# Performance work log

Hardware: AMD Instinct MI355X
Metric: run time of the kernel (lower is better)

The kernel has to match this reference:

```python
import jax, jax.numpy as jnp
import numpy as np

D_MODEL, D_K, D_V, H = 1024, 64, 64, 16
B, NQ, NK = 4, 2048, 2048


def setup_inputs() -> dict:
    key = jax.random.key(0)
    ks = jax.random.split(key, 14)
    def xavier(k, fan_in, fan_out):
        lim = np.sqrt(6.0 / (fan_in + fan_out))
        return jax.random.uniform(k, (fan_in, fan_out), jnp.float32, -lim, lim)
    return {
        "queries": jax.random.normal(ks[0], (B, NQ, D_MODEL), jnp.float32),
        "keys": jax.random.normal(ks[1], (B, NK, D_MODEL), jnp.float32),
        "values": jax.random.normal(ks[2], (B, NK, D_MODEL), jnp.float32),
        "language_feature": jax.random.normal(ks[3], (B, NQ, D_MODEL), jnp.float32),
        "Wq": xavier(ks[4], D_MODEL, H * D_K), "bq": jnp.zeros((H * D_K,), jnp.float32),
        "Wk": xavier(ks[5], D_MODEL, H * D_K), "bk": jnp.zeros((H * D_K,), jnp.float32),
        "Wv": xavier(ks[6], D_MODEL, H * D_V), "bv": jnp.zeros((H * D_V,), jnp.float32),
        "Ws": xavier(ks[7], D_MODEL, H * D_K), "bs": jnp.zeros((H * D_K,), jnp.float32),
        "Wo": xavier(ks[8], H * D_V, D_MODEL), "bo": jnp.zeros((D_MODEL,), jnp.float32),
    }


def reference(queries, keys, values, language_feature, Wq, bq, Wk, bk, Wv, bv, Ws, bs, Wo, bo):
    b, nq = queries.shape[:2]
    nk = keys.shape[1]
    scale = 1.0 / np.sqrt(D_K)
    # projections -> [b, h, n, d]
    q = (queries @ Wq + bq).reshape(b, nq, H, D_K).transpose(0, 2, 1, 3)
    s = (language_feature @ Ws + bs).reshape(b, nq, H, D_K).transpose(0, 2, 1, 3)
    k = (keys @ Wk + bk).reshape(b, nk, H, D_K).transpose(0, 2, 1, 3)
    v = (values @ Wv + bv).reshape(b, nk, H, D_V).transpose(0, 2, 1, 3)
    # raw scaled scores [b, h, nq, nk]
    att = jnp.einsum("bhqd,bhkd->bhqk", q, k) * scale
    # language branch: per-query dot(q_i, s_i) -> [b, h, nq]
    lang = jnp.einsum("bhqd,bhqd->bhq", q, s) * scale
    # concatenated softmax over [nk + 1]; only last column (beta) is used
    combined = jax.nn.softmax(jnp.concatenate([att, lang[..., None]], axis=-1), axis=-1)
    beta = combined[..., -1:]  # [b, h, nq, 1]
    # NOTE: original uses RAW (non-softmaxed) att for the value aggregation
    att_v = jnp.einsum("bhqk,bhkd->bhqd", att, v)
    out = beta * s + (1.0 - beta) * att_v  # [b, h, nq, d]
    out = out.transpose(0, 2, 1, 3).reshape(b, nq, H * D_V)
    return out @ Wo + bo
```

## Files before the change

kernel.cpp:

```cpp
#include <hip/hip_runtime.h>


#define SCALE 0.125f
#define LOG2E 1.44269504088896f
#define SCLOG 0.18033688011112042f

typedef __attribute__((ext_vector_type(8))) short bf16x8;
typedef __attribute__((ext_vector_type(4))) short s16x4;
typedef __attribute__((ext_vector_type(4))) float f32x4;

__device__ __forceinline__ float b2f(short x) {
  return __uint_as_float(((unsigned)(unsigned short)x) << 16);
}
__device__ __forceinline__ short f2b(float x) {
  unsigned u = __float_as_uint(x);
  unsigned r = (u + 0x7fffu + ((u >> 16) & 1u)) >> 16;
  return (short)r;
}
__device__ __forceinline__ float fexp2(float x) {
  float r;
  asm("v_exp_f32 %0, %1" : "=v"(r) : "v"(x));
  return r;
}

__device__ __forceinline__ void gl2lds16(const short* g, short* l) {
  __builtin_amdgcn_global_load_lds(
      (const __attribute__((address_space(1))) unsigned int*)g,
      (__attribute__((address_space(3))) unsigned int*)l, 16, 0, 0);
}

__global__ __launch_bounds__(256) void a2b_kernel(const float* I0, const float* I1,
                                                  const float* I2, const float* I3,
                                                  short* O0, short* O1, short* O2, short* O3) {
  const float* Ip[4] = {I0, I1, I2, I3};
  short* Op[4] = {O0, O1, O2, O3};
  const float* I = Ip[blockIdx.z];
  short* O = Op[blockIdx.z];
  const size_t n = (size_t)8192 * 1024;
  size_t stride = (size_t)gridDim.x * 256 * 8;
  for (size_t i = ((size_t)blockIdx.x * 256 + threadIdx.x) * 8; i < n; i += stride) {
    f32x4 v0 = *reinterpret_cast<const f32x4*>(&I[i]);
    f32x4 v1 = *reinterpret_cast<const f32x4*>(&I[i + 4]);
    bf16x8 o;
    for (int j = 0; j < 4; ++j) { o[j] = f2b(v0[j]); o[j + 4] = f2b(v1[j]); }
    *reinterpret_cast<bf16x8*>(&O[i]) = o;
  }
}

__global__ __launch_bounds__(256) void wtrans_kernel(
    const float* W0, const float* W1, const float* W2, const float* W3, const float* W4,
    short* O0, short* O1, short* O2, short* O3, short* O4) {
  const float* Wp[5] = {W0, W1, W2, W3, W4};
  short* Op[5] = {O0, O1, O2, O3, O4};
  const float* W = Wp[blockIdx.z];
  short* O = Op[blockIdx.z];
  int n0 = blockIdx.x * 64, k0 = blockIdx.y * 64;
  __shared__ float ts[64 * 68];
  int tid = threadIdx.x;
  int r = tid >> 4, c = (tid & 15) * 4;
  for (int ir = 0; ir < 4; ++ir) {
    f32x4 v = *reinterpret_cast<const f32x4*>(&W[(size_t)(k0 + r + ir * 16) * 1024 + n0 + c]);
    *reinterpret_cast<f32x4*>(&ts[(r + ir * 16) * 68 + c]) = v;
  }
  __syncthreads();
  for (int ir = 0; ir < 4; ++ir) {
    int n = r + ir * 16;
    s16x4 o;
    for (int j = 0; j < 4; ++j) o[j] = f2b(ts[(c + j) * 68 + n]);
    *reinterpret_cast<s16x4*>(&O[(size_t)(n0 + n) * 1024 + k0 + c]) = o;
  }
}

#define GEMM_STAGE_HALF(T, HALF)                                            \
  {                                                                         \
    int kst = (T) * 32;                                                     \
    int sb = (T) & 3;                                                       \
    short* Ad = &AsAll[sb * 8192];                                          \
    short* Bd = &BsAll[sb * 8192];                                          \
    int s = tid + (HALF) * 512;                                             \
    int row = s >> 2, cc = s & 3;                                           \
    int gc = (cc ^ ((row >> 1) & 3)) * 8;                                   \
    gl2lds16(&Ag[(size_t)(m0 + row) * 1024 + kst + gc], &Ad[s * 8]);        \
    gl2lds16(&Bg[(size_t)(n0 + row) * 1024 + kst + gc], &Bd[s * 8]);        \
  }

#define GEMM_STAGE(T) { GEMM_STAGE_HALF(T, 0); GEMM_STAGE_HALF(T, 1); }

#define GEMM_BODY(T, DO_STAGE, VM)                                          \
  {                                                                         \
    const int bi = (T) & 3;                                                 \
    const short* Ab = &AsAll[bi * 8192];                                    \
    const short* Bb = &BsAll[bi * 8192];                                    \
    bf16x8 a[4], b[4];                                                      \
    _Pragma("unroll") for (int i = 0; i < 4; ++i) {                         \
      int r = wr + i * 16 + lr;                                             \
      a[i] = *reinterpret_cast<const bf16x8*>(                              \
          &Ab[r * 32 + ((lg ^ ((r >> 1) & 3)) * 8)]);                       \
    }                                                                       \
    _Pragma("unroll") for (int j = 0; j < 4; ++j) {                         \
      int rn = wc + j * 16 + lr;                                            \
      b[j] = *reinterpret_cast<const bf16x8*>(                              \
          &Bb[rn * 32 + ((lg ^ ((rn >> 1) & 3)) * 8)]);                     \
    }                                                                       \
    if (DO_STAGE) GEMM_STAGE_HALF((T) + 3, 0);                              \
    __builtin_amdgcn_s_setprio(1);                                          \
    _Pragma("unroll") for (int j = 0; j < 4; ++j)                           \
      _Pragma("unroll") for (int i = 0; i < 4; ++i)                         \
        acc[i][j] = __builtin_amdgcn_mfma_f32_16x16x32_bf16(a[i], b[j], acc[i][j], 0, 0, 0); \
    __builtin_amdgcn_s_setprio(0);                                          \
    __builtin_amdgcn_s_barrier();                                           \
    bf16x8 a2[4];                                                           \
    _Pragma("unroll") for (int i = 0; i < 4; ++i) {                         \
      int r = wr + 64 + i * 16 + lr;                                        \
      a2[i] = *reinterpret_cast<const bf16x8*>(                             \
          &Ab[r * 32 + ((lg ^ ((r >> 1) & 3)) * 8)]);                       \
    }                                                                       \
    if (DO_STAGE) GEMM_STAGE_HALF((T) + 3, 1);                              \
    asm volatile("s_waitcnt vmcnt(" #VM ")" ::: "memory");                  \
    __builtin_amdgcn_s_setprio(1);                                          \
    _Pragma("unroll") for (int j = 0; j < 4; ++j)                           \
      _Pragma("unroll") for (int i = 0; i < 4; ++i)                         \
        acc[i + 4][j] = __builtin_amdgcn_mfma_f32_16x16x32_bf16(a2[i], b[j], acc[i + 4][j], 0, 0, 0); \
    __builtin_amdgcn_s_setprio(0);                                          \
    __builtin_amdgcn_s_barrier();                                           \
  }

#define GEMM_CORE()                                                         \
  GEMM_STAGE(0); GEMM_STAGE(1); GEMM_STAGE(2);                              \
  asm volatile("s_waitcnt vmcnt(8)" ::: "memory");                          \
  __builtin_amdgcn_s_barrier();                                             \
  for (int t = 0; t < 29; ++t) GEMM_BODY(t, true, 8);                       \
  GEMM_BODY(29, false, 4);                                                  \
  GEMM_BODY(30, false, 0);                                                  \
  GEMM_BODY(31, false, 0);

__global__ __launch_bounds__(512, 2) void proj_gemm_kernel(
    const short* A0, const short* A1, const short* A2, const short* A3,
    const short* W0, const short* W1, const short* W2, const short* W3,
    const float* c0, const float* c1, const float* c2, const float* c3,
    short* O0, short* O1, short* O2, short* O3) {
  const short* Ap[4] = {A0, A1, A2, A3};
  const short* Wp[4] = {W0, W1, W2, W3};
  const float* bp[4] = {c0, c1, c2, c3};
  short* Op[4] = {O0, O1, O2, O3};

  int id = blockIdx.x;
  int work = (id & 7) * 64 + (id >> 3);
  int z = work >> 7;
  int rem = work & 127;
  int my = rem >> 2;
  int nx = rem & 3;
  const short* Ag = Ap[z];
  const short* Bg = Wp[z];
  const float* bias = bp[z];
  short* Out = Op[z];
  int m0 = my * 256, n0 = nx * 256;

  __shared__ short AsAll[4 * 8192];
  __shared__ short BsAll[4 * 8192];
  int tid = threadIdx.x;
  int wave = tid >> 6, lane = tid & 63, lg = lane >> 4, lr = lane & 15;
  int wr = (wave >> 2) * 128, wc = (wave & 3) * 64;

  f32x4 acc[8][4] = {};

  GEMM_CORE();

#pragma unroll
  for (int j = 0; j < 4; ++j) {
    int n = n0 + wc + j * 16 + lr;
    float bi = bias[n];
    int hh = n >> 6, d = n & 63;
#pragma unroll
    for (int i = 0; i < 8; ++i)
      for (int rr = 0; rr < 4; ++rr) {
        int m = m0 + wr + i * 16 + lg * 4 + rr;
        int bb = m >> 11, t = m & 2047;
        Out[(size_t)(((bb << 4) + hh) * 2048 + t) * 64 + d] = f2b(acc[i][j][rr] + bi);
      }
  }
}

__global__ __launch_bounds__(256) void final_gemm_kernel(const short* A, const short* Wt,
                                                         const float* bias, float* Out) {
  int id = blockIdx.x;
  int work = (id & 7) * 64 + (id >> 3);
  int my = work >> 3, nx = work & 7;
  int m0 = my * 128, n0 = nx * 128;

  __shared__ short As[128 * 64];
  __shared__ short Bs[128 * 64];
  int tid = threadIdx.x;
  int wave = tid >> 6, lane = tid & 63, lg = lane >> 4, lr = lane & 15;
  int wr = (wave >> 1) * 64, wc = (wave & 1) * 64;
  f32x4 acc[4][4] = {};
  int srow = lane >> 3, scol = (lane & 7) * 8;

  for (int k0 = 0; k0 < 1024; k0 += 64) {
    __syncthreads();
#pragma unroll
    for (int i = 0; i < 4; ++i) {
      int c = i * 4 + wave;
      gl2lds16(&A[(size_t)(m0 + c * 8 + srow) * 1024 + k0 + scol], &As[c * 512 + lane * 8]);
      gl2lds16(&Wt[(size_t)(n0 + c * 8 + srow) * 1024 + k0 + scol], &Bs[c * 512 + lane * 8]);
    }
    __syncthreads();
#pragma unroll
    for (int kk = 0; kk < 2; ++kk) {
      bf16x8 a[4], b[4];
      for (int i = 0; i < 4; ++i)
        a[i] = *reinterpret_cast<const bf16x8*>(&As[(wr + i * 16 + lr) * 64 + kk * 32 + lg * 8]);
      for (int j = 0; j < 4; ++j)
        b[j] = *reinterpret_cast<const bf16x8*>(&Bs[(wc + j * 16 + lr) * 64 + kk * 32 + lg * 8]);
      for (int i = 0; i < 4; ++i)
        for (int j = 0; j < 4; ++j)
          acc[i][j] = __builtin_amdgcn_mfma_f32_16x16x32_bf16(a[i], b[j], acc[i][j], 0, 0, 0);
    }
  }
  for (int j = 0; j < 4; ++j) {
    int n = n0 + wc + j * 16 + lr;
    float bi = bias[n];
    for (int i = 0; i < 4; ++i)
      for (int rr = 0; rr < 4; ++rr) {
        int m = m0 + wr + i * 16 + lg * 4 + rr;
        Out[(size_t)m * 1024 + n] = acc[i][j][rr] + bi;
      }
  }
}

__global__ __launch_bounds__(256) void kv_kernel(const short* Kp, const short* Vp, float* KVp) {
  int c = blockIdx.x, bh = blockIdx.y;
  int tid = threadIdx.x;
  __shared__ float Ks[32 * 64];
  __shared__ float Vs[32 * 64];
  int srow = tid >> 3, scol = (tid & 7) * 8;
  int dk = tid >> 2, dv0 = (tid & 3) * 16;
  float acc[16] = {};
  for (int sub = 0; sub < 8; ++sub) {
    int tkb = c * 256 + sub * 32;
    __syncthreads();
    bf16x8 kv = *reinterpret_cast<const bf16x8*>(&Kp[(size_t)(bh * 2048 + tkb + srow) * 64 + scol]);
    bf16x8 vv = *reinterpret_cast<const bf16x8*>(&Vp[(size_t)(bh * 2048 + tkb + srow) * 64 + scol]);
    for (int j = 0; j < 8; ++j) {
      Ks[srow * 64 + scol + j] = b2f(kv[j]);
      Vs[srow * 64 + scol + j] = b2f(vv[j]);
    }
    __syncthreads();
    for (int tok = 0; tok < 32; ++tok) {
      float kval = Ks[tok * 64 + dk];
#pragma unroll
      for (int j = 0; j < 16; ++j) acc[j] += kval * Vs[tok * 64 + dv0 + j];
    }
  }
  float* o = &KVp[(size_t)(bh * 8 + c) * 4096 + dk * 64 + dv0];
  for (int j = 0; j < 16; ++j) o[j] = acc[j];
}

__global__ __launch_bounds__(256) void kvred_kernel(const float* KVp, short* KVt) {
  int bh = blockIdx.x;
  for (int e = threadIdx.x; e < 4096; e += 256) {
    float s = 0.f;
    for (int cc = 0; cc < 8; ++cc) s += KVp[(size_t)(bh * 8 + cc) * 4096 + e];
    int dk = e >> 6, dv = e & 63;
    KVt[(size_t)bh * 4096 + dv * 64 + dk] = f2b(s);
  }
}

__global__ __launch_bounds__(256) void beta_combine_kernel(
    const short* Qp, const short* Kp, const short* Sp, const short* KVt, short* X) {
  int bh = blockIdx.y, q0 = blockIdx.x * 64;
  int b = bh >> 4, h = bh & 15;
  int tid = threadIdx.x;
  __shared__ float lsm[64];
  __shared__ short Ks[2][64 * 64];

  {
    int row = tid >> 2, seg = tid & 3;
    const short* qr = Qp + (size_t)(bh * 2048 + q0 + row) * 64 + seg * 16;
    const short* sr = Sp + (size_t)(bh * 2048 + q0 + row) * 64 + seg * 16;
    float sum = 0.f;
    for (int cc = 0; cc < 2; ++cc) {
      bf16x8 qv = reinterpret_cast<const bf16x8*>(qr)[cc];
      bf16x8 sv = reinterpret_cast<const bf16x8*>(sr)[cc];
      for (int j = 0; j < 8; ++j) sum += b2f(qv[j]) * b2f(sv[j]);
    }
    sum += __shfl_xor(sum, 1);
    sum += __shfl_xor(sum, 2);
    if (seg == 0) lsm[row] = sum * SCLOG;
  }
  __syncthreads();

  int wave = tid >> 6, lane = tid & 63, lg = lane >> 4, lr = lane & 15;
  int qrow = q0 + wave * 16 + lr;
  const bf16x8* qbase = reinterpret_cast<const bf16x8*>(Qp + (size_t)(bh * 2048 + qrow) * 64);
  bf16x8 a0 = qbase[lg];
  bf16x8 a1 = qbase[4 + lg];
  bf16x8 as0, as1;
#pragma unroll
  for (int j = 0; j < 8; ++j) {
    as0[j] = f2b(b2f(a0[j]) * SCLOG);
    as1[j] = f2b(b2f(a1[j]) * SCLOG);
  }
  const short* Kb = Kp + (size_t)bh * 2048 * 64;

  int srow = tid >> 3, schunk = tid & 7;
  int sxor = (schunk ^ (srow & 7)) * 8;

  gl2lds16(&Kb[(size_t)srow * 64 + sxor], &Ks[0][tid * 8]);
  gl2lds16(&Kb[(size_t)(srow + 32) * 64 + sxor], &Ks[0][2048 + tid * 8]);

  float s0 = 0.f, s1 = 0.f, s2 = 0.f, s3 = 0.f;
  for (int t = 0; t < 32; ++t) {
    __builtin_amdgcn_s_barrier();
    if (t < 31) {
      const short* src = Kb + (size_t)(t + 1) * 4096;
      short* dst = &Ks[(t + 1) & 1][0];
      gl2lds16(&src[(size_t)srow * 64 + sxor], &dst[tid * 8]);
      gl2lds16(&src[(size_t)(srow + 32) * 64 + sxor], &dst[2048 + tid * 8]);
      asm volatile("s_waitcnt vmcnt(2)" ::: "memory");
    } else {
      asm volatile("s_waitcnt vmcnt(0)" ::: "memory");
    }
    __builtin_amdgcn_s_barrier();
    __builtin_amdgcn_sched_barrier(0);
    const short* Kbuf = &Ks[t & 1][0];
    f32x4 sc[4];
#pragma unroll
    for (int nt = 0; nt < 4; ++nt) {
      int row = nt * 16 + lr;
      int xs = row & 7;
      bf16x8 b0 = *reinterpret_cast<const bf16x8*>(&Kbuf[row * 64 + ((lg ^ xs) * 8)]);
      bf16x8 b1 = *reinterpret_cast<const bf16x8*>(&Kbuf[row * 64 + (((4 + lg) ^ xs) * 8)]);
      f32x4 z = {0.f, 0.f, 0.f, 0.f};
      z = __builtin_amdgcn_mfma_f32_16x16x32_bf16(as0, b0, z, 0, 0, 0);
      z = __builtin_amdgcn_mfma_f32_16x16x32_bf16(as1, b1, z, 0, 0, 0);
      sc[nt] = z;
    }
#pragma unroll
    for (int nt = 0; nt < 4; ++nt) {
      s0 += fexp2(sc[nt][0]);
      s1 += fexp2(sc[nt][1]);
      s2 += fexp2(sc[nt][2]);
      s3 += fexp2(sc[nt][3]);
    }
  }
  for (int m = 1; m < 16; m <<= 1) {
    s0 += __shfl_xor(s0, m);
    s1 += __shfl_xor(s1, m);
    s2 += __shfl_xor(s2, m);
    s3 += __shfl_xor(s3, m);
  }
  float bt[4];
  {
    float sarr[4] = {s0, s1, s2, s3};
#pragma unroll
    for (int rr = 0; rr < 4; ++rr) {
      int rl = wave * 16 + lg * 4 + rr;
      float el = fexp2(lsm[rl]);
      bt[rr] = el / (sarr[rr] + el);
    }
  }
  const short* kvb = KVt + (size_t)bh * 4096;
#pragma unroll
  for (int nt = 0; nt < 4; ++nt) {
    const bf16x8* bb8 = reinterpret_cast<const bf16x8*>(&kvb[(nt * 16 + lr) * 64]);
    bf16x8 b0 = bb8[lg], b1 = bb8[4 + lg];
    f32x4 z = {0.f, 0.f, 0.f, 0.f};
    z = __builtin_amdgcn_mfma_f32_16x16x32_bf16(a0, b0, z, 0, 0, 0);
    z = __builtin_amdgcn_mfma_f32_16x16x32_bf16(a1, b1, z, 0, 0, 0);
#pragma unroll
    for (int rr = 0; rr < 4; ++rr) {
      int rl = wave * 16 + lg * 4 + rr;
      int q = q0 + rl;
      float sv = b2f(Sp[(size_t)(bh * 2048 + q) * 64 + nt * 16 + lr]);
      float val = bt[rr] * sv + (1.0f - bt[rr]) * (SCALE * z[rr]);
      X[(size_t)(b * 2048 + q) * 1024 + h * 64 + nt * 16 + lr] = f2b(val);
    }
  }
}

extern "C" void kernel_launch(void* const* d_in, const int* in_sizes, int n_in,
                              void* d_out, int out_size, void* d_ws, size_t ws_size,
                              hipStream_t stream) {
  const float* queries = (const float*)d_in[0];
  const float* keys = (const float*)d_in[1];
  const float* values = (const float*)d_in[2];
  const float* langf = (const float*)d_in[3];
  const float* Wq = (const float*)d_in[4];
  const float* bq = (const float*)d_in[5];
  const float* Wk = (const float*)d_in[6];
  const float* bk = (const float*)d_in[7];
  const float* Wv = (const float*)d_in[8];
  const float* bv = (const float*)d_in[9];
  const float* Ws = (const float*)d_in[10];
  const float* bs = (const float*)d_in[11];
  const float* Wo = (const float*)d_in[12];
  const float* bo = (const float*)d_in[13];
  float* out = (float*)d_out;

  char* ws = (char*)d_ws;
  const size_t MB = 1ull << 20;
  short* Wqt = (short*)(ws + 0 * MB);
  short* Wkt = (short*)(ws + 2 * MB);
  short* Wvt = (short*)(ws + 4 * MB);
  short* Wst = (short*)(ws + 6 * MB);
  short* Wot = (short*)(ws + 8 * MB);
  short* Qp = (short*)(ws + 10 * MB);
  short* Kp = (short*)(ws + 26 * MB);
  short* Vp = (short*)(ws + 42 * MB);
  short* Sp = (short*)(ws + 58 * MB);
  short* X = (short*)(ws + 74 * MB);
  float* KVp = (float*)(ws + 90 * MB);
  short* KVt = (short*)(ws + 98 * MB);
  short* Qb = (short*)(ws + 100 * MB);
  short* Kb = (short*)(ws + 116 * MB);
  short* Vb = (short*)(ws + 132 * MB);
  short* Lb = (short*)(ws + 148 * MB);

  a2b_kernel<<<dim3(512, 1, 4), 256, 0, stream>>>(queries, keys, values, langf, Qb, Kb, Vb, Lb);
  wtrans_kernel<<<dim3(16, 16, 5), 256, 0, stream>>>(Wq, Wk, Wv, Ws, Wo, Wqt, Wkt, Wvt, Wst, Wot);
  proj_gemm_kernel<<<512, 512, 0, stream>>>(Qb, Kb, Vb, Lb, Wqt, Wkt, Wvt, Wst,
                                            bq, bk, bv, bs, Qp, Kp, Vp, Sp);
  kv_kernel<<<dim3(8, 64), 256, 0, stream>>>(Kp, Vp, KVp);
  kvred_kernel<<<64, 256, 0, stream>>>(KVp, KVt);
  beta_combine_kernel<<<dim3(32, 64), 256, 0, stream>>>(Qp, Kp, Sp, KVt, X);
  final_gemm_kernel<<<512, 256, 0, stream>>>(X, Wot, bo, out);
}
```

Before: 261.6 us.

## Fuse fp32-to-bf16 activation conversion into projection GEMM A-tile loading

Removes the separate a2b conversion kernel. The projection GEMM now loads fp32 activations into registers, converts them with packed bf16 conversion instructions and writes them to a double-buffered LDS A tile, while B keeps async global-to-LDS loads with triple buffering. This drops a full write and reread of four 8192x1024 bf16 tensors, but adds register pressure, fp32 global traffic inside the GEMM and a shallower prefetch pipeline. The kv_kernel's LDS reads and writes are also vectorized.

```diff
diff --git a/kernel.cpp b/kernel.cpp
--- a/kernel.cpp
+++ b/kernel.cpp
@@ -22,29 +22,21 @@
   asm("v_exp_f32 %0, %1" : "=v"(r) : "v"(x));
   return r;
 }
+__device__ __forceinline__ bf16x8 cvt8(f32x4 lo, f32x4 hi) {
+  unsigned u0, u1, u2, u3;
+  asm("v_cvt_pk_bf16_f32 %0, %1, %2" : "=v"(u0) : "v"(lo[0]), "v"(lo[1]));
+  asm("v_cvt_pk_bf16_f32 %0, %1, %2" : "=v"(u1) : "v"(lo[2]), "v"(lo[3]));
+  asm("v_cvt_pk_bf16_f32 %0, %1, %2" : "=v"(u2) : "v"(hi[0]), "v"(hi[1]));
+  asm("v_cvt_pk_bf16_f32 %0, %1, %2" : "=v"(u3) : "v"(hi[2]), "v"(hi[3]));
+  union { unsigned u[4]; bf16x8 v; } r;
+  r.u[0] = u0; r.u[1] = u1; r.u[2] = u2; r.u[3] = u3;
+  return r.v;
+}
 
 __device__ __forceinline__ void gl2lds16(const short* g, short* l) {
   __builtin_amdgcn_global_load_lds(
       (const __attribute__((address_space(1))) unsigned int*)g,
       (__attribute__((address_space(3))) unsigned int*)l, 16, 0, 0);
-}
-
-__global__ __launch_bounds__(256) void a2b_kernel(const float* I0, const float* I1,
-                                                  const float* I2, const float* I3,
-                                                  short* O0, short* O1, short* O2, short* O3) {
-  const float* Ip[4] = {I0, I1, I2, I3};
-  short* Op[4] = {O0, O1, O2, O3};
-  const float* I = Ip[blockIdx.z];
-  short* O = Op[blockIdx.z];
-  const size_t n = (size_t)8192 * 1024;
-  size_t stride = (size_t)gridDim.x * 256 * 8;
-  for (size_t i = ((size_t)blockIdx.x * 256 + threadIdx.x) * 8; i < n; i += stride) {
-    f32x4 v0 = *reinterpret_cast<const f32x4*>(&I[i]);
-    f32x4 v1 = *reinterpret_cast<const f32x4*>(&I[i + 4]);
-    bf16x8 o;
-    for (int j = 0; j < 4; ++j) { o[j] = f2b(v0[j]); o[j + 4] = f2b(v1[j]); }
-    *reinterpret_cast<bf16x8*>(&O[i]) = o;
-  }
 }
 
 __global__ __launch_bounds__(256) void wtrans_kernel(
@@ -71,26 +63,45 @@
   }
 }
 
-#define GEMM_STAGE_HALF(T, HALF)                                            \
+
+#define A_LOAD(T, R0, R1, R2, R3)                                           \
   {                                                                         \
     int kst = (T) * 32;                                                     \
-    int sb = (T) & 3;                                                       \
-    short* Ad = &AsAll[sb * 8192];                                          \
-    short* Bd = &BsAll[sb * 8192];                                          \
-    int s = tid + (HALF) * 512;                                             \
-    int row = s >> 2, cc = s & 3;                                           \
-    int gc = (cc ^ ((row >> 1) & 3)) * 8;                                   \
-    gl2lds16(&Ag[(size_t)(m0 + row) * 1024 + kst + gc], &Ad[s * 8]);        \
-    gl2lds16(&Bg[(size_t)(n0 + row) * 1024 + kst + gc], &Bd[s * 8]);        \
-  }
-
-#define GEMM_STAGE(T) { GEMM_STAGE_HALF(T, 0); GEMM_STAGE_HALF(T, 1); }
-
-#define GEMM_BODY(T, DO_STAGE, VM)                                          \
+    int row0 = tid >> 2, cc0 = tid & 3;                                     \
+    int gc0 = (cc0 ^ ((row0 >> 1) & 3)) * 8;                                \
+    const float* ap0 = &Ag[(size_t)(m0 + row0) * 1024 + kst + gc0];         \
+    R0 = *reinterpret_cast<const f32x4*>(ap0);                              \
+    R1 = *reinterpret_cast<const f32x4*>(ap0 + 4);                          \
+    int row1 = row0 + 128;                                                  \
+    int gc1 = (cc0 ^ ((row1 >> 1) & 3)) * 8;                                \
+    const float* ap1 = &Ag[(size_t)(m0 + row1) * 1024 + kst + gc1];         \
+    R2 = *reinterpret_cast<const f32x4*>(ap1);                              \
+    R3 = *reinterpret_cast<const f32x4*>(ap1 + 4);                          \
+  }
+
+#define A_WRITE(T, R0, R1, R2, R3)                                          \
   {                                                                         \
-    const int bi = (T) & 3;                                                 \
-    const short* Ab = &AsAll[bi * 8192];                                    \
-    const short* Bb = &BsAll[bi * 8192];                                    \
+    short* Ad = &As[(T) & 1][0];                                            \
+    *reinterpret_cast<bf16x8*>(&Ad[tid * 8]) = cvt8(R0, R1);                \
+    *reinterpret_cast<bf16x8*>(&Ad[(tid + 512) * 8]) = cvt8(R2, R3);        \
+  }
+
+#define B_STAGE(T)                                                          \
+  {                                                                         \
+    int kst = (T) * 32;                                                     \
+    short* Bd = &Bs[(T) % 3][0];                                            \
+    _Pragma("unroll") for (int it = 0; it < 2; ++it) {                      \
+      int s = tid + it * 512;                                               \
+      int row = s >> 2, cc = s & 3;                                         \
+      int gc = (cc ^ ((row >> 1) & 3)) * 8;                                 \
+      gl2lds16(&Bg[(size_t)(n0 + row) * 1024 + kst + gc], &Bd[s * 8]);      \
+    }                                                                       \
+  }
+
+#define BODY(T, DO_STAGE, VM, DO_WRITE, C0, C1, C2, C3, N0, N1, N2, N3)     \
+  {                                                                         \
+    const short* Ab = &As[(T) & 1][0];                                      \
+    const short* Bb = &Bs[(T) % 3][0];                                      \
     bf16x8 a[4], b[4];                                                      \
     _Pragma("unroll") for (int i = 0; i < 4; ++i) {                         \
       int r = wr + i * 16 + lr;                                             \
@@ -102,7 +113,7 @@
       b[j] = *reinterpret_cast<const bf16x8*>(                              \
           &Bb[rn * 32 + ((lg ^ ((rn >> 1) & 3)) * 8)]);                     \
     }                                                                       \
-    if (DO_STAGE) GEMM_STAGE_HALF((T) + 3, 0);                              \
+    if (DO_STAGE) { B_STAGE((T) + 2); A_LOAD((T) + 2, N0, N1, N2, N3); }    \
     __builtin_amdgcn_s_setprio(1);                                          \
     _Pragma("unroll") for (int j = 0; j < 4; ++j)                           \
       _Pragma("unroll") for (int i = 0; i < 4; ++i)                         \
@@ -115,31 +126,40 @@
       a2[i] = *reinterpret_cast<const bf16x8*>(                             \
           &Ab[r * 32 + ((lg ^ ((r >> 1) & 3)) * 8)]);                       \
     }                                                                       \
-    if (DO_STAGE) GEMM_STAGE_HALF((T) + 3, 1);                              \
     asm volatile("s_waitcnt vmcnt(" #VM ")" ::: "memory");                  \
+    if (DO_WRITE) A_WRITE((T) + 1, C0, C1, C2, C3);                         \
     __builtin_amdgcn_s_setprio(1);                                          \
     _Pragma("unroll") for (int j = 0; j < 4; ++j)                           \
       _Pragma("unroll") for (int i = 0; i < 4; ++i)                         \
         acc[i + 4][j] = __builtin_amdgcn_mfma_f32_16x16x32_bf16(a2[i], b[j], acc[i + 4][j], 0, 0, 0); \
     __builtin_amdgcn_s_setprio(0);                                          \
+    asm volatile("s_waitcnt lgkmcnt(0)" ::: "memory");                      \
     __builtin_amdgcn_s_barrier();                                           \
   }
 
 #define GEMM_CORE()                                                         \
-  GEMM_STAGE(0); GEMM_STAGE(1); GEMM_STAGE(2);                              \
-  asm volatile("s_waitcnt vmcnt(8)" ::: "memory");                          \
+  f32x4 p0, p1, p2, p3, q0, q1, q2, q3;                                     \
+  B_STAGE(0); A_LOAD(0, p0, p1, p2, p3);                                    \
+  B_STAGE(1); A_LOAD(1, q0, q1, q2, q3);                                    \
+  asm volatile("s_waitcnt vmcnt(6)" ::: "memory");                          \
+  A_WRITE(0, p0, p1, p2, p3);                                               \
+  asm volatile("s_waitcnt lgkmcnt(0)" ::: "memory");                        \
   __builtin_amdgcn_s_barrier();                                             \
-  for (int t = 0; t < 29; ++t) GEMM_BODY(t, true, 8);                       \
-  GEMM_BODY(29, false, 4);                                                  \
-  GEMM_BODY(30, false, 0);                                                  \
-  GEMM_BODY(31, false, 0);
+  for (int t = 0; t < 28; t += 2) {                                         \
+    BODY(t, true, 6, true, q0, q1, q2, q3, p0, p1, p2, p3);                 \
+    BODY(t + 1, true, 6, true, p0, p1, p2, p3, q0, q1, q2, q3);             \
+  }                                                                         \
+  BODY(28, true, 6, true, q0, q1, q2, q3, p0, p1, p2, p3);                  \
+  BODY(29, true, 6, true, p0, p1, p2, p3, q0, q1, q2, q3);                  \
+  BODY(30, false, 0, true, q0, q1, q2, q3, p0, p1, p2, p3);                 \
+  BODY(31, false, 0, false, p0, p1, p2, p3, q0, q1, q2, q3);
 
 __global__ __launch_bounds__(512, 2) void proj_gemm_kernel(
-    const short* A0, const short* A1, const short* A2, const short* A3,
+    const float* A0, const float* A1, const float* A2, const float* A3,
     const short* W0, const short* W1, const short* W2, const short* W3,
     const float* c0, const float* c1, const float* c2, const float* c3,
     short* O0, short* O1, short* O2, short* O3) {
-  const short* Ap[4] = {A0, A1, A2, A3};
+  const float* Ap[4] = {A0, A1, A2, A3};
   const short* Wp[4] = {W0, W1, W2, W3};
   const float* bp[4] = {c0, c1, c2, c3};
   short* Op[4] = {O0, O1, O2, O3};
@@ -150,14 +170,14 @@
   int rem = work & 127;
   int my = rem >> 2;
   int nx = rem & 3;
-  const short* Ag = Ap[z];
+  const float* Ag = Ap[z];
   const short* Bg = Wp[z];
   const float* bias = bp[z];
   short* Out = Op[z];
   int m0 = my * 256, n0 = nx * 256;
 
-  __shared__ short AsAll[4 * 8192];
-  __shared__ short BsAll[4 * 8192];
+  __shared__ short As[2][8192];
+  __shared__ short Bs[3][8192];
   int tid = threadIdx.x;
   int wave = tid >> 6, lane = tid & 63, lg = lane >> 4, lr = lane & 15;
   int wr = (wave >> 2) * 128, wc = (wave & 3) * 64;
@@ -188,8 +208,8 @@
   int my = work >> 3, nx = work & 7;
   int m0 = my * 128, n0 = nx * 128;
 
-  __shared__ short As[128 * 64];
-  __shared__ short Bs[128 * 64];
+  __shared__ short Asl[128 * 64];
+  __shared__ short Bsl[128 * 64];
   int tid = threadIdx.x;
   int wave = tid >> 6, lane = tid & 63, lg = lane >> 4, lr = lane & 15;
   int wr = (wave >> 1) * 64, wc = (wave & 1) * 64;
@@ -201,17 +221,17 @@
 #pragma unroll
     for (int i = 0; i < 4; ++i) {
       int c = i * 4 + wave;
-      gl2lds16(&A[(size_t)(m0 + c * 8 + srow) * 1024 + k0 + scol], &As[c * 512 + lane * 8]);
-      gl2lds16(&Wt[(size_t)(n0 + c * 8 + srow) * 1024 + k0 + scol], &Bs[c * 512 + lane * 8]);
+      gl2lds16(&A[(size_t)(m0 + c * 8 + srow) * 1024 + k0 + scol], &Asl[c * 512 + lane * 8]);
+      gl2lds16(&Wt[(size_t)(n0 + c * 8 + srow) * 1024 + k0 + scol], &Bsl[c * 512 + lane * 8]);
     }
     __syncthreads();
 #pragma unroll
     for (int kk = 0; kk < 2; ++kk) {
       bf16x8 a[4], b[4];
       for (int i = 0; i < 4; ++i)
-        a[i] = *reinterpret_cast<const bf16x8*>(&As[(wr + i * 16 + lr) * 64 + kk * 32 + lg * 8]);
+        a[i] = *reinterpret_cast<const bf16x8*>(&Asl[(wr + i * 16 + lr) * 64 + kk * 32 + lg * 8]);
       for (int j = 0; j < 4; ++j)
-        b[j] = *reinterpret_cast<const bf16x8*>(&Bs[(wc + j * 16 + lr) * 64 + kk * 32 + lg * 8]);
+        b[j] = *reinterpret_cast<const bf16x8*>(&Bsl[(wc + j * 16 + lr) * 64 + kk * 32 + lg * 8]);
       for (int i = 0; i < 4; ++i)
         for (int j = 0; j < 4; ++j)
           acc[i][j] = __builtin_amdgcn_mfma_f32_16x16x32_bf16(a[i], b[j], acc[i][j], 0, 0, 0);
@@ -241,15 +261,30 @@
     __syncthreads();
     bf16x8 kv = *reinterpret_cast<const bf16x8*>(&Kp[(size_t)(bh * 2048 + tkb + srow) * 64 + scol]);
     bf16x8 vv = *reinterpret_cast<const bf16x8*>(&Vp[(size_t)(bh * 2048 + tkb + srow) * 64 + scol]);
-    for (int j = 0; j < 8; ++j) {
-      Ks[srow * 64 + scol + j] = b2f(kv[j]);
-      Vs[srow * 64 + scol + j] = b2f(vv[j]);
-    }
+    f32x4 ka, kb, va, vb;
+#pragma unroll
+    for (int j = 0; j < 4; ++j) {
+      ka[j] = b2f(kv[j]); kb[j] = b2f(kv[j + 4]);
+      va[j] = b2f(vv[j]); vb[j] = b2f(vv[j + 4]);
+    }
+    *reinterpret_cast<f32x4*>(&Ks[srow * 64 + scol]) = ka;
+    *reinterpret_cast<f32x4*>(&Ks[srow * 64 + scol + 4]) = kb;
+    *reinterpret_cast<f32x4*>(&Vs[srow * 64 + scol]) = va;
+    *reinterpret_cast<f32x4*>(&Vs[srow * 64 + scol + 4]) = vb;
     __syncthreads();
     for (int tok = 0; tok < 32; ++tok) {
       float kval = Ks[tok * 64 + dk];
-#pragma unroll
-      for (int j = 0; j < 16; ++j) acc[j] += kval * Vs[tok * 64 + dv0 + j];
+      f32x4 v0 = *reinterpret_cast<const f32x4*>(&Vs[tok * 64 + dv0]);
+      f32x4 v1 = *reinterpret_cast<const f32x4*>(&Vs[tok * 64 + dv0 + 4]);
+      f32x4 v2 = *reinterpret_cast<const f32x4*>(&Vs[tok * 64 + dv0 + 8]);
+      f32x4 v3 = *reinterpret_cast<const f32x4*>(&Vs[tok * 64 + dv0 + 12]);
+#pragma unroll
+      for (int j = 0; j < 4; ++j) {
+        acc[j] += kval * v0[j];
+        acc[4 + j] += kval * v1[j];
+        acc[8 + j] += kval * v2[j];
+        acc[12 + j] += kval * v3[j];
+      }
     }
   }
   float* o = &KVp[(size_t)(bh * 8 + c) * 4096 + dk * 64 + dv0];
@@ -412,15 +447,11 @@
   short* X = (short*)(ws + 74 * MB);
   float* KVp = (float*)(ws + 90 * MB);
   short* KVt = (short*)(ws + 98 * MB);
-  short* Qb = (short*)(ws + 100 * MB);
-  short* Kb = (short*)(ws + 116 * MB);
-  short* Vb = (short*)(ws + 132 * MB);
-  short* Lb = (short*)(ws + 148 * MB);
-
-  a2b_kernel<<<dim3(512, 1, 4), 256, 0, stream>>>(queries, keys, values, langf, Qb, Kb, Vb, Lb);
+
   wtrans_kernel<<<dim3(16, 16, 5), 256, 0, stream>>>(Wq, Wk, Wv, Ws, Wo, Wqt, Wkt, Wvt, Wst, Wot);
-  proj_gemm_kernel<<<512, 512, 0, stream>>>(Qb, Kb, Vb, Lb, Wqt, Wkt, Wvt, Wst,
-                                            bq, bk, bv, bs, Qp, Kp, Vp, Sp);
+  proj_gemm_kernel<<<512, 512, 0, stream>>>(queries, keys, values, langf,
+                                            Wqt, Wkt, Wvt, Wst, bq, bk, bv, bs,
+                                            Qp, Kp, Vp, Sp);
   kv_kernel<<<dim3(8, 64), 256, 0, stream>>>(Kp, Vp, KVp);
   kvred_kernel<<<64, 256, 0, stream>>>(KVp, KVt);
   beta_combine_kernel<<<dim3(32, 64), 256, 0, stream>>>(Qp, Kp, Sp, KVt, X);
```

Measured after the change: 233.7 us. 1.12x faster.
